# Kernel tuning notes

Hardware: AMD Instinct MI355X
Metric: run time of the kernel (lower is better)

## Reference

```python
import jax, jax.numpy as jnp
import numpy as np
from jax.scipy.special import logsumexp

EPSILON = 0.01        # temperature
DIST_THRESH = 0.2
NUM_ITERS = 3
NEG_INF = -1.0e9

B, N, M, C = 4, 4096, 4096, 256


def setup_inputs() -> dict:
    key = jax.random.key(0)
    k1, k2, k3, k4, k5 = jax.random.split(key, 5)
    source_feats = jax.random.normal(k1, (B, N, C), dtype=jnp.float32)
    source_locs = jax.random.uniform(k2, (B, N, 2), dtype=jnp.float32)
    target_locs = jax.random.uniform(k3, (B, M, 2), dtype=jnp.float32)
    source_valid_mask = jax.random.bernoulli(k4, 0.9, (B, N))
    target_valid_mask = jax.random.bernoulli(k5, 0.9, (B, M))
    return {
        "source_feats": source_feats,
        "source_locs": source_locs,
        "target_locs": target_locs,
        "source_valid_mask": source_valid_mask,
        "target_valid_mask": target_valid_mask,
    }


def reference(source_feats, source_locs, target_locs, source_valid_mask, target_valid_mask):
    # pairwise squared distances: [B, M, N]
    diff = target_locs[:, :, None, :] - source_locs[:, None, :, :]  # [B, M, N, 2]
    dist_sq = jnp.sum(diff * diff, axis=-1)                          # [B, M, N]
    log_K = -dist_sq / (EPSILON + 1e-8)

    valid_connection = dist_sq < (DIST_THRESH ** 2)
    valid_connection = valid_connection & source_valid_mask[:, None, :]
    valid_connection = valid_connection & target_valid_mask[:, :, None]
    log_K = jnp.where(valid_connection, log_K, NEG_INF)

    # Sinkhorn iterations in log space
    v = jnp.zeros((log_K.shape[0], 1, log_K.shape[2]), dtype=log_K.dtype)  # [B,1,N]
    u = jnp.zeros((log_K.shape[0], log_K.shape[1], 1), dtype=log_K.dtype)  # [B,M,1]
    for _ in range(NUM_ITERS):
        u = -logsumexp(log_K + v, axis=2, keepdims=True)
        v = -logsumexp(log_K + u, axis=1, keepdims=True)
        v = jnp.where(source_valid_mask[:, None, :], v, 0.0)

    attn = jnp.exp(log_K + u + v)  # [B, M, N]
    attn = jax.lax.stop_gradient(attn)  # original computes it under torch.no_grad

    target_feats = jnp.einsum('bmn,bnc->bmc', attn, source_feats)
    target_feats = target_feats * target_valid_mask[:, :, None].astype(target_feats.dtype)
    has_source = jnp.any(valid_connection, axis=-1, keepdims=True)
    target_feats = target_feats * has_source.astype(target_feats.dtype)
    return target_feats
```

## Files before the change

kernel.cpp:

```cpp
#include <hip/hip_runtime.h>
#include <math.h>

#define BB 4
#define BN 4096
#define CC 256
constexpr float T2      = 0.04f;
constexpr float INV_EPS = (float)(1.0 / 0.01000001);

typedef __attribute__((ext_vector_type(8)))  short bf16x8;
typedef __attribute__((ext_vector_type(16))) float f32x16;

__device__ __forceinline__ int cell_of(float x, float y) {
  int cx = (int)(x * 5.0f); cx = cx < 0 ? 0 : (cx > 4 ? 4 : cx);
  int cy = (int)(y * 5.0f); cy = cy < 0 ? 0 : (cy > 4 ? 4 : cy);
  return cy * 5 + cx;
}

__global__ __launch_bounds__(256) void k_bin(
    const float* __restrict__ tlocs, const float* __restrict__ slocs,
    const int* __restrict__ tmask, const int* __restrict__ smask,
    int* __restrict__ Zc, int* __restrict__ qcnt,
    int* __restrict__ starts_t, int* __restrict__ starts_s,
    int* __restrict__ perm_t, int* __restrict__ perm_s,
    float4* __restrict__ t_sorted, float4* __restrict__ s_sorted) {
  const int which = blockIdx.x & 1, b = blockIdx.x >> 1;
  const float* locs = which ? slocs : tlocs;
  const int*   mask = which ? smask : tmask;
  int* starts       = which ? starts_s : starts_t;
  int* perm         = which ? perm_s : perm_t;
  float4* pack      = which ? s_sorted : t_sorted;
  const int tid = threadIdx.x;
  if (blockIdx.x == 0) {
    Zc[tid] = 0;
    if (tid == 0) qcnt[0] = 0;
  }
  __shared__ int cnt[25];
  __shared__ int st[26];
  __shared__ int cur[25];
  if (tid < 25) cnt[tid] = 0;
  __syncthreads();
  for (int i = tid; i < BN; i += 256)
    atomicAdd(&cnt[cell_of(locs[(b * BN + i) * 2], locs[(b * BN + i) * 2 + 1])], 1);
  __syncthreads();
  if (tid == 0) {
    int acc = 0;
    for (int c = 0; c < 25; c++) { st[c] = acc; acc += cnt[c]; }
    st[25] = acc;
  }
  __syncthreads();
  if (tid < 25) cur[tid] = st[tid];
  if (tid < 26) starts[b * 32 + tid] = st[tid];
  __syncthreads();
  for (int i = tid; i < BN; i += 256) {
    float x = locs[(b * BN + i) * 2], y = locs[(b * BN + i) * 2 + 1];
    int pos = atomicAdd(&cur[cell_of(x, y)], 1);
    perm[b * BN + pos] = i;
    pack[b * BN + pos] = make_float4(x, y, 0.f, mask[b * BN + i] ? 1.f : 0.f);
  }
}

__global__ __launch_bounds__(256) void k_pack(
    const float* __restrict__ feats, const int* __restrict__ perm_s,
    unsigned* __restrict__ fB) {
  const int b   = blockIdx.x >> 8;
  const int blk = blockIdx.x & 255;
  const int tid = threadIdx.x;
  __shared__ int sidx[16];
  if (tid < 16) sidx[tid] = perm_s[b * BN + blk * 16 + tid];
  __syncthreads();
  const int ch = tid;
  unsigned pk[16];
  #pragma unroll
  for (int sl = 0; sl < 16; sl++) {
    float f = feats[((((size_t)(b << 12)) + sidx[sl]) << 8) + ch];
    unsigned fbt = __float_as_uint(f);
    unsigned hb  = fbt & 0xFFFF0000u;
    float lo = f - __uint_as_float(hb);
    pk[sl] = hb | (__float_as_uint(lo) >> 16);
  }
  unsigned* dst = fB + ((((size_t)b << 8) + blk) << 12) + ch * 16;
  #pragma unroll
  for (int q = 0; q < 4; q++)
    ((uint4*)dst)[q] = make_uint4(pk[q*4], pk[q*4+1], pk[q*4+2], pk[q*4+3]);
}

__global__ __launch_bounds__(256) void k_sink(const float4* __restrict__ opp,
                                              float4* __restrict__ own,
                                              const int* __restrict__ opp_starts,
                                              const int* __restrict__ Zin,
                                              int* __restrict__ Zout,
                                              int zero_invalid) {
  const int wv   = threadIdx.x >> 6;
  const int lane = threadIdx.x & 63;
  const int rowb = blockIdx.x * 16 + wv * 4;
  const int b    = rowb >> 12;
  float4 me[4];
  float  s[4] = {0.f, 0.f, 0.f, 0.f};
  int ryLo = 5, ryHi = -1, rxLo = 5, rxHi = -1;
  #pragma unroll
  for (int i = 0; i < 4; i++) {
    me[i] = own[rowb + i];
    if (me[i].w != 0.f) {
      int cell = cell_of(me[i].x, me[i].y);
      int cy = cell / 5, cx = cell % 5;
      ryLo = min(ryLo, max(cy - 1, 0)); ryHi = max(ryHi, min(cy + 1, 4));
      rxLo = min(rxLo, max(cx - 1, 0)); rxHi = max(rxHi, min(cx + 1, 4));
    }
  }
  for (int ry = ryLo; ry <= ryHi; ry++) {
    const int r0 = opp_starts[b * 32 + ry * 5 + rxLo];
    const int r1 = opp_starts[b * 32 + ry * 5 + rxHi + 1];
    for (int j = r0 + lane; j < r1; j += 64) {
      float4 o = opp[b * BN + j];
      #pragma unroll
      for (int i = 0; i < 4; i++) {
        float dx = me[i].x - o.x, dy = me[i].y - o.y;
        float d2 = fmaf(dx, dx, dy * dy);
        bool  c  = (d2 < T2) && (o.w != 0.f) && (me[i].w != 0.f);
        float t  = c ? fmaf(d2, -INV_EPS, o.z) : -3e30f;
        s[i] += __expf(t);
      }
    }
  }
  #pragma unroll
  for (int i = 0; i < 4; i++)
    for (int off = 32; off > 0; off >>= 1) s[i] += __shfl_xor(s[i], off);
  if (lane == 0) {
    const float Zf = (float)Zin[b];
    #pragma unroll
    for (int i = 0; i < 4; i++) {
      float ss  = s[i] + Zf;
      float val = (ss > 0.f) ? -logf(ss) : 1.0e9f;
      if (zero_invalid && me[i].w == 0.f) val = 0.f;
      own[rowb + i] = make_float4(me[i].x, me[i].y, val, me[i].w);
      if (val == 1.0e9f) atomicAdd(&Zout[b], 1);
    }
  }
}

#define NITEMS (BB * 25 * 12)

__global__ __launch_bounds__(256, 4) void k_out(
    const unsigned* __restrict__ fB, const float4* __restrict__ t_sorted,
    const float4* __restrict__ s_sorted, const int* __restrict__ perm_t,
    const int* __restrict__ starts_t, const int* __restrict__ starts_s,
    int* __restrict__ qcnt, float* __restrict__ out) {
  __shared__ float4 tL[32];
  __shared__ __align__(16) float Dl[32 * 268];
  __shared__ int qi;

  const int tid  = threadIdx.x;
  const int lane = tid & 63;
  const int w    = tid >> 6;
  const int kg   = lane >> 5;
  const int ln   = lane & 31;

  for (;;) {
    if (tid == 0) qi = atomicAdd(qcnt, 1);
    __syncthreads();
    const int item = qi;
    __syncthreads();
    if (item >= NITEMS) break;
    const int b    = item / 300;
    const int r1_  = item % 300;
    const int cell = r1_ / 12;
    const int chunk = r1_ % 12;
    const int cy = cell / 5, cx = cell % 5;
    const int t0 = starts_t[b * 32 + cell], t1 = starts_t[b * 32 + cell + 1];
    const int base = t0 + chunk * 32;
    if (base >= t1) continue;
    const int ry0 = max(cy - 1, 0), ry1 = min(cy + 1, 4);
    const int rx0 = max(cx - 1, 0), rx1 = min(cx + 1, 4);
    const int nt = min(32, t1 - base);

    if (tid < 32)
      tL[tid] = (tid < nt) ? t_sorted[b * BN + base + tid]
                           : make_float4(0.f, 0.f, 0.f, 0.f);
    __syncthreads();
    const float4 t4a = tL[ln];
    const int sB = b * BN;
    const unsigned* fBb = fB + (((size_t)b) << 20);
    const int aoff0 = (w * 64 + ln) * 16 + kg * 8;
    const int aoff1 = aoff0 + 512;

    f32x16 acc0, acc1;
    #pragma unroll
    for (int i = 0; i < 16; i++) { acc0[i] = 0.f; acc1[i] = 0.f; }

    for (int ry = ry0; ry <= ry1; ry++) {
      const int s0 = starts_s[b * 32 + ry * 5 + rx0];
      const int s1 = starts_s[b * 32 + ry * 5 + rx1 + 1];
      if (s0 >= s1) continue;
      const int blk0 = s0 >> 4;
      const int nBlk = ((s1 + 15) >> 4) - blk0;

      const unsigned* g0p = fBb + ((size_t)blk0 << 12);
      uint4 cA00 = *(const uint4*)(g0p + aoff0);
      uint4 cA01 = *(const uint4*)(g0p + aoff0 + 4);
      uint4 cA10 = *(const uint4*)(g0p + aoff1);
      uint4 cA11 = *(const uint4*)(g0p + aoff1 + 4);

      for (int r = 0; r < nBlk; r++) {
        const int tn = blk0 + min(r + 1, nBlk - 1);
        const unsigned* gn = fBb + ((size_t)tn << 12);
        uint4 nA00 = *(const uint4*)(gn + aoff0);
        uint4 nA01 = *(const uint4*)(gn + aoff0 + 4);
        uint4 nA10 = *(const uint4*)(gn + aoff1);
        uint4 nA11 = *(const uint4*)(gn + aoff1 + 4);
        const int j0 = (blk0 + r) * 16 + kg * 8;
        float4 s4v[8];
        #pragma unroll
        for (int e = 0; e < 8; e++)
          s4v[e] = s_sorted[sB + j0 + e];
        union { unsigned u[4]; bf16x8 v; } BH, BL;
        #pragma unroll
        for (int i = 0; i < 4; i++) {
          unsigned hh[2], ll[2];
          #pragma unroll
          for (int p = 0; p < 2; p++) {
            const int e = 2 * i + p;
            float4 s4 = s4v[e];
            int j = j0 + e;
            float dx = t4a.x - s4.x, dy = t4a.y - s4.y;
            float d2 = fmaf(dx, dx, dy * dy);
            bool  c  = (j >= s0) && (j < s1) && (d2 < T2) &&
                       (s4.w != 0.f) && (t4a.w != 0.f);
            float a  = c ? __expf(fmaf(d2, -INV_EPS, t4a.z + s4.z)) : 0.f;
            unsigned ab = __float_as_uint(a);
            unsigned hb = ab & 0xFFFF0000u;
            float alo = a - __uint_as_float(hb);
            hh[p] = ab >> 16;
            ll[p] = __float_as_uint(alo) >> 16;
          }
          BH.u[i] = hh[0] | (hh[1] << 16);
          BL.u[i] = ll[0] | (ll[1] << 16);
        }
        #pragma unroll
        for (int mt = 0; mt < 2; mt++) {
          union { uint4 q[2]; unsigned u[8]; } A;
          A.q[0] = (mt == 0) ? cA00 : cA10;
          A.q[1] = (mt == 0) ? cA01 : cA11;
          union { unsigned u[4]; bf16x8 v; } AH, AL;
          #pragma unroll
          for (int i = 0; i < 4; i++) {
            AH.u[i] = (A.u[2*i] >> 16)     | (A.u[2*i+1] & 0xFFFF0000u);
            AL.u[i] = (A.u[2*i] & 0xFFFFu) | (A.u[2*i+1] << 16);
          }
          if (mt == 0) {
            acc0 = __builtin_amdgcn_mfma_f32_32x32x16_bf16(AH.v, BH.v, acc0, 0, 0, 0);
            acc0 = __builtin_amdgcn_mfma_f32_32x32x16_bf16(AH.v, BL.v, acc0, 0, 0, 0);
            acc0 = __builtin_amdgcn_mfma_f32_32x32x16_bf16(AL.v, BH.v, acc0, 0, 0, 0);
          } else {
            acc1 = __builtin_amdgcn_mfma_f32_32x32x16_bf16(AH.v, BH.v, acc1, 0, 0, 0);
            acc1 = __builtin_amdgcn_mfma_f32_32x32x16_bf16(AH.v, BL.v, acc1, 0, 0, 0);
            acc1 = __builtin_amdgcn_mfma_f32_32x32x16_bf16(AL.v, BH.v, acc1, 0, 0, 0);
          }
        }
        cA00 = nA00; cA01 = nA01; cA10 = nA10; cA11 = nA11;
      }
    }

    __syncthreads();
    #pragma unroll
    for (int mt = 0; mt < 2; mt++) {
      #pragma unroll
      for (int rg = 0; rg < 4; rg++) {
        int chb = w * 64 + mt * 32 + 8 * rg + 4 * kg;
        float4 v;
        if (mt == 0) v = make_float4(acc0[rg*4], acc0[rg*4+1], acc0[rg*4+2], acc0[rg*4+3]);
        else         v = make_float4(acc1[rg*4], acc1[rg*4+1], acc1[rg*4+2], acc1[rg*4+3]);
        *(float4*)&Dl[ln * 268 + chb] = v;
      }
    }
    __syncthreads();
    {
      const int tmg = tid >> 5, chg = tid & 31;
      #pragma unroll
      for (int i = 0; i < 4; i++) {
        int tm = tmg * 4 + i;
        if (tm < nt) {
          int row = perm_t[sB + base + tm];
          float* op = out + (((b << 12) + row) << 8) + chg * 4;
          *(float4*)(op)       = *(float4*)&Dl[tm * 268 + chg * 4];
          *(float4*)(op + 128) = *(float4*)&Dl[tm * 268 + 128 + chg * 4];
        }
      }
    }
  }
}

extern "C" void kernel_launch(void* const* d_in, const int* in_sizes, int n_in,
                              void* d_out, int out_size, void* d_ws, size_t ws_size,
                              hipStream_t stream) {
  const float* feats = (const float*)d_in[0];
  const float* slocs = (const float*)d_in[1];
  const float* tlocs = (const float*)d_in[2];
  const int*   smask = (const int*)d_in[3];
  const int*   tmask = (const int*)d_in[4];
  float* out = (float*)d_out;

  char* ws = (char*)d_ws;
  int*    qcnt     = (int*)(ws);
  int*    Zc       = (int*)(ws + 1024);
  int*    starts_t = (int*)(ws + 2048);
  int*    starts_s = (int*)(ws + 2560);
  int*    perm_t   = (int*)(ws + 4096);
  int*    perm_s   = (int*)(ws + 69632);
  float4* s_sorted = (float4*)(ws + 135168);
  float4* t_sorted = (float4*)(ws + 397312);
  unsigned* fB     = (unsigned*)(ws + 663552);

  hipMemsetAsync(out, 0, (size_t)out_size * sizeof(float), stream);
  k_bin<<<8, 256, 0, stream>>>(tlocs, slocs, tmask, smask, Zc, qcnt,
                               starts_t, starts_s, perm_t, perm_s,
                               t_sorted, s_sorted);
  k_pack<<<1024, 256, 0, stream>>>(feats, perm_s, fB);
  for (int it = 0; it < 3; it++) {
    k_sink<<<1024, 256, 0, stream>>>(s_sorted, t_sorted, starts_s,
                                     Zc + (it == 0 ? 0 : (2 * it) * 4),
                                     Zc + (2 * it + 1) * 4, 0);
    k_sink<<<1024, 256, 0, stream>>>(t_sorted, s_sorted, starts_t,
                                     Zc + (2 * it + 1) * 4,
                                     Zc + (2 * it + 2) * 4, 1);
  }
  k_out<<<1024, 256, 0, stream>>>(fB, t_sorted, s_sorted, perm_t,
                                  starts_t, starts_s, qcnt, out);
}
```

Baseline: 535.1 us.

## Replace atomic work queue in k_out with static grid and halve LDS staging

```diff
diff --git a/kernel.cpp b/kernel.cpp
--- a/kernel.cpp
+++ b/kernel.cpp
@@ -19,7 +19,7 @@
 __global__ __launch_bounds__(256) void k_bin(
     const float* __restrict__ tlocs, const float* __restrict__ slocs,
     const int* __restrict__ tmask, const int* __restrict__ smask,
-    int* __restrict__ Zc, int* __restrict__ qcnt,
+    int* __restrict__ Zc,
     int* __restrict__ starts_t, int* __restrict__ starts_s,
     int* __restrict__ perm_t, int* __restrict__ perm_s,
     float4* __restrict__ t_sorted, float4* __restrict__ s_sorted) {
@@ -30,10 +30,7 @@
   int* perm         = which ? perm_s : perm_t;
   float4* pack      = which ? s_sorted : t_sorted;
   const int tid = threadIdx.x;
-  if (blockIdx.x == 0) {
-    Zc[tid] = 0;
-    if (tid == 0) qcnt[0] = 0;
-  }
+  if (blockIdx.x == 0) Zc[tid] = 0;
   __shared__ int cnt[25];
   __shared__ int st[26];
   __shared__ int cur[25];
@@ -140,14 +137,13 @@
 
 #define NITEMS (BB * 25 * 12)
 
-__global__ __launch_bounds__(256, 4) void k_out(
+__global__ __launch_bounds__(256, 6) void k_out(
     const unsigned* __restrict__ fB, const float4* __restrict__ t_sorted,
     const float4* __restrict__ s_sorted, const int* __restrict__ perm_t,
     const int* __restrict__ starts_t, const int* __restrict__ starts_s,
-    int* __restrict__ qcnt, float* __restrict__ out) {
+    float* __restrict__ out) {
   __shared__ float4 tL[32];
-  __shared__ __align__(16) float Dl[32 * 268];
-  __shared__ int qi;
+  __shared__ __align__(16) float Dl[32 * 132];
 
   const int tid  = threadIdx.x;
   const int lane = tid & 63;
@@ -155,121 +151,120 @@
   const int kg   = lane >> 5;
   const int ln   = lane & 31;
 
-  for (;;) {
-    if (tid == 0) qi = atomicAdd(qcnt, 1);
-    __syncthreads();
-    const int item = qi;
-    __syncthreads();
-    if (item >= NITEMS) break;
-    const int b    = item / 300;
-    const int r1_  = item % 300;
-    const int cell = r1_ / 12;
-    const int chunk = r1_ % 12;
-    const int cy = cell / 5, cx = cell % 5;
-    const int t0 = starts_t[b * 32 + cell], t1 = starts_t[b * 32 + cell + 1];
-    const int base = t0 + chunk * 32;
-    if (base >= t1) continue;
-    const int ry0 = max(cy - 1, 0), ry1 = min(cy + 1, 4);
-    const int rx0 = max(cx - 1, 0), rx1 = min(cx + 1, 4);
-    const int nt = min(32, t1 - base);
-
-    if (tid < 32)
-      tL[tid] = (tid < nt) ? t_sorted[b * BN + base + tid]
-                           : make_float4(0.f, 0.f, 0.f, 0.f);
-    __syncthreads();
-    const float4 t4a = tL[ln];
-    const int sB = b * BN;
-    const unsigned* fBb = fB + (((size_t)b) << 20);
-    const int aoff0 = (w * 64 + ln) * 16 + kg * 8;
-    const int aoff1 = aoff0 + 512;
-
-    f32x16 acc0, acc1;
-    #pragma unroll
-    for (int i = 0; i < 16; i++) { acc0[i] = 0.f; acc1[i] = 0.f; }
-
-    for (int ry = ry0; ry <= ry1; ry++) {
-      const int s0 = starts_s[b * 32 + ry * 5 + rx0];
-      const int s1 = starts_s[b * 32 + ry * 5 + rx1 + 1];
-      if (s0 >= s1) continue;
-      const int blk0 = s0 >> 4;
-      const int nBlk = ((s1 + 15) >> 4) - blk0;
-
-      const unsigned* g0p = fBb + ((size_t)blk0 << 12);
-      uint4 cA00 = *(const uint4*)(g0p + aoff0);
-      uint4 cA01 = *(const uint4*)(g0p + aoff0 + 4);
-      uint4 cA10 = *(const uint4*)(g0p + aoff1);
-      uint4 cA11 = *(const uint4*)(g0p + aoff1 + 4);
-
-      for (int r = 0; r < nBlk; r++) {
-        const int tn = blk0 + min(r + 1, nBlk - 1);
-        const unsigned* gn = fBb + ((size_t)tn << 12);
-        uint4 nA00 = *(const uint4*)(gn + aoff0);
-        uint4 nA01 = *(const uint4*)(gn + aoff0 + 4);
-        uint4 nA10 = *(const uint4*)(gn + aoff1);
-        uint4 nA11 = *(const uint4*)(gn + aoff1 + 4);
-        const int j0 = (blk0 + r) * 16 + kg * 8;
-        float4 s4v[8];
+  const int item = blockIdx.x;
+  const int b    = item / 300;
+  const int r1_  = item % 300;
+  const int cell = r1_ / 12;
+  const int chunk = r1_ % 12;
+  const int cy = cell / 5, cx = cell % 5;
+  const int t0 = starts_t[b * 32 + cell], t1 = starts_t[b * 32 + cell + 1];
+  const int base = t0 + chunk * 32;
+  if (base >= t1) return;
+  const int ry0 = max(cy - 1, 0), ry1 = min(cy + 1, 4);
+  const int rx0 = max(cx - 1, 0), rx1 = min(cx + 1, 4);
+  const int nt = min(32, t1 - base);
+
+  if (tid < 32)
+    tL[tid] = (tid < nt) ? t_sorted[b * BN + base + tid]
+                         : make_float4(0.f, 0.f, 0.f, 0.f);
+  __syncthreads();
+  const float4 t4a = tL[ln];
+  const int sB = b * BN;
+  const unsigned* fBb = fB + (((size_t)b) << 20);
+  const int aoff0 = (w * 64 + ln) * 16 + kg * 8;
+  const int aoff1 = aoff0 + 512;
+
+  f32x16 acc0, acc1;
+  #pragma unroll
+  for (int i = 0; i < 16; i++) { acc0[i] = 0.f; acc1[i] = 0.f; }
+
+  for (int ry = ry0; ry <= ry1; ry++) {
+    const int s0 = starts_s[b * 32 + ry * 5 + rx0];
+    const int s1 = starts_s[b * 32 + ry * 5 + rx1 + 1];
+    if (s0 >= s1) continue;
+    const int blk0 = s0 >> 4;
+    const int nBlk = ((s1 + 15) >> 4) - blk0;
+
+    const unsigned* g0p = fBb + ((size_t)blk0 << 12);
+    uint4 cA00 = *(const uint4*)(g0p + aoff0);
+    uint4 cA01 = *(const uint4*)(g0p + aoff0 + 4);
+    uint4 cA10 = *(const uint4*)(g0p + aoff1);
+    uint4 cA11 = *(const uint4*)(g0p + aoff1 + 4);
+
+    for (int r = 0; r < nBlk; r++) {
+      const int tn = blk0 + min(r + 1, nBlk - 1);
+      const unsigned* gn = fBb + ((size_t)tn << 12);
+      uint4 nA00 = *(const uint4*)(gn + aoff0);
+      uint4 nA01 = *(const uint4*)(gn + aoff0 + 4);
+      uint4 nA10 = *(const uint4*)(gn + aoff1);
+      uint4 nA11 = *(const uint4*)(gn + aoff1 + 4);
+      const int j0 = (blk0 + r) * 16 + kg * 8;
+      float4 s4v[8];
+      #pragma unroll
+      for (int e = 0; e < 8; e++)
+        s4v[e] = s_sorted[sB + j0 + e];
+      union { unsigned u[4]; bf16x8 v; } BH, BL;
+      #pragma unroll
+      for (int i = 0; i < 4; i++) {
+        unsigned hh[2], ll[2];
         #pragma unroll
-        for (int e = 0; e < 8; e++)
-          s4v[e] = s_sorted[sB + j0 + e];
-        union { unsigned u[4]; bf16x8 v; } BH, BL;
+        for (int p = 0; p < 2; p++) {
+          const int e = 2 * i + p;
+          float4 s4 = s4v[e];
+          int j = j0 + e;
+          float dx = t4a.x - s4.x, dy = t4a.y - s4.y;
+          float d2 = fmaf(dx, dx, dy * dy);
+          bool  c  = (j >= s0) && (j < s1) && (d2 < T2) &&
+                     (s4.w != 0.f) && (t4a.w != 0.f);
+          float a  = c ? __expf(fmaf(d2, -INV_EPS, t4a.z + s4.z)) : 0.f;
+          unsigned ab = __float_as_uint(a);
+          unsigned hb = ab & 0xFFFF0000u;
+          float alo = a - __uint_as_float(hb);
+          hh[p] = ab >> 16;
+          ll[p] = __float_as_uint(alo) >> 16;
+        }
+        BH.u[i] = hh[0] | (hh[1] << 16);
+        BL.u[i] = ll[0] | (ll[1] << 16);
+      }
+      #pragma unroll
+      for (int mt = 0; mt < 2; mt++) {
+        union { uint4 q[2]; unsigned u[8]; } A;
+        A.q[0] = (mt == 0) ? cA00 : cA10;
+        A.q[1] = (mt == 0) ? cA01 : cA11;
+        union { unsigned u[4]; bf16x8 v; } AH, AL;
         #pragma unroll
         for (int i = 0; i < 4; i++) {
-          unsigned hh[2], ll[2];
-          #pragma unroll
-          for (int p = 0; p < 2; p++) {
-            const int e = 2 * i + p;
-            float4 s4 = s4v[e];
-            int j = j0 + e;
-            float dx = t4a.x - s4.x, dy = t4a.y - s4.y;
-            float d2 = fmaf(dx, dx, dy * dy);
-            bool  c  = (j >= s0) && (j < s1) && (d2 < T2) &&
-                       (s4.w != 0.f) && (t4a.w != 0.f);
-            float a  = c ? __expf(fmaf(d2, -INV_EPS, t4a.z + s4.z)) : 0.f;
-            unsigned ab = __float_as_uint(a);
-            unsigned hb = ab & 0xFFFF0000u;
-            float alo = a - __uint_as_float(hb);
-            hh[p] = ab >> 16;
-            ll[p] = __float_as_uint(alo) >> 16;
-          }
-          BH.u[i] = hh[0] | (hh[1] << 16);
-          BL.u[i] = ll[0] | (ll[1] << 16);
-        }
+          AH.u[i] = (A.u[2*i] >> 16)     | (A.u[2*i+1] & 0xFFFF0000u);
+          AL.u[i] = (A.u[2*i] & 0xFFFFu) | (A.u[2*i+1] << 16);
+        }
+        if (mt == 0) {
+          acc0 = __builtin_amdgcn_mfma_f32_32x32x16_bf16(AH.v, BH.v, acc0, 0, 0, 0);
+          acc0 = __builtin_amdgcn_mfma_f32_32x32x16_bf16(AH.v, BL.v, acc0, 0, 0, 0);
+          acc0 = __builtin_amdgcn_mfma_f32_32x32x16_bf16(AL.v, BH.v, acc0, 0, 0, 0);
+        } else {
+          acc1 = __builtin_amdgcn_mfma_f32_32x32x16_bf16(AH.v, BH.v, acc1, 0, 0, 0);
+          acc1 = __builtin_amdgcn_mfma_f32_32x32x16_bf16(AH.v, BL.v, acc1, 0, 0, 0);
+          acc1 = __builtin_amdgcn_mfma_f32_32x32x16_bf16(AL.v, BH.v, acc1, 0, 0, 0);
+        }
+      }
+      cA00 = nA00; cA01 = nA01; cA10 = nA10; cA11 = nA11;
+    }
+  }
+
+  #pragma unroll
+  for (int p = 0; p < 2; p++) {
+    __syncthreads();
+    if ((w >> 1) == p) {
+      #pragma unroll
+      for (int mt = 0; mt < 2; mt++) {
         #pragma unroll
-        for (int mt = 0; mt < 2; mt++) {
-          union { uint4 q[2]; unsigned u[8]; } A;
-          A.q[0] = (mt == 0) ? cA00 : cA10;
-          A.q[1] = (mt == 0) ? cA01 : cA11;
-          union { unsigned u[4]; bf16x8 v; } AH, AL;
-          #pragma unroll
-          for (int i = 0; i < 4; i++) {
-            AH.u[i] = (A.u[2*i] >> 16)     | (A.u[2*i+1] & 0xFFFF0000u);
-            AL.u[i] = (A.u[2*i] & 0xFFFFu) | (A.u[2*i+1] << 16);
-          }
-          if (mt == 0) {
-            acc0 = __builtin_amdgcn_mfma_f32_32x32x16_bf16(AH.v, BH.v, acc0, 0, 0, 0);
-            acc0 = __builtin_amdgcn_mfma_f32_32x32x16_bf16(AH.v, BL.v, acc0, 0, 0, 0);
-            acc0 = __builtin_amdgcn_mfma_f32_32x32x16_bf16(AL.v, BH.v, acc0, 0, 0, 0);
-          } else {
-            acc1 = __builtin_amdgcn_mfma_f32_32x32x16_bf16(AH.v, BH.v, acc1, 0, 0, 0);
-            acc1 = __builtin_amdgcn_mfma_f32_32x32x16_bf16(AH.v, BL.v, acc1, 0, 0, 0);
-            acc1 = __builtin_amdgcn_mfma_f32_32x32x16_bf16(AL.v, BH.v, acc1, 0, 0, 0);
-          }
-        }
-        cA00 = nA00; cA01 = nA01; cA10 = nA10; cA11 = nA11;
-      }
-    }
-
-    __syncthreads();
-    #pragma unroll
-    for (int mt = 0; mt < 2; mt++) {
-      #pragma unroll
-      for (int rg = 0; rg < 4; rg++) {
-        int chb = w * 64 + mt * 32 + 8 * rg + 4 * kg;
-        float4 v;
-        if (mt == 0) v = make_float4(acc0[rg*4], acc0[rg*4+1], acc0[rg*4+2], acc0[rg*4+3]);
-        else         v = make_float4(acc1[rg*4], acc1[rg*4+1], acc1[rg*4+2], acc1[rg*4+3]);
-        *(float4*)&Dl[ln * 268 + chb] = v;
+        for (int rg = 0; rg < 4; rg++) {
+          int chb = (w & 1) * 64 + mt * 32 + 8 * rg + 4 * kg;
+          float4 v;
+          if (mt == 0) v = make_float4(acc0[rg*4], acc0[rg*4+1], acc0[rg*4+2], acc0[rg*4+3]);
+          else         v = make_float4(acc1[rg*4], acc1[rg*4+1], acc1[rg*4+2], acc1[rg*4+3]);
+          *(float4*)&Dl[ln * 132 + chb] = v;
+        }
       }
     }
     __syncthreads();
@@ -280,9 +275,8 @@
         int tm = tmg * 4 + i;
         if (tm < nt) {
           int row = perm_t[sB + base + tm];
-          float* op = out + (((b << 12) + row) << 8) + chg * 4;
-          *(float4*)(op)       = *(float4*)&Dl[tm * 268 + chg * 4];
-          *(float4*)(op + 128) = *(float4*)&Dl[tm * 268 + 128 + chg * 4];
+          float* op = out + (((b << 12) + row) << 8) + p * 128 + chg * 4;
+          *(float4*)op = *(float4*)&Dl[tm * 132 + chg * 4];
         }
       }
     }
@@ -300,7 +294,6 @@
   float* out = (float*)d_out;
 
   char* ws = (char*)d_ws;
-  int*    qcnt     = (int*)(ws);
   int*    Zc       = (int*)(ws + 1024);
   int*    starts_t = (int*)(ws + 2048);
   int*    starts_s = (int*)(ws + 2560);
@@ -311,7 +304,7 @@
   unsigned* fB     = (unsigned*)(ws + 663552);
 
   hipMemsetAsync(out, 0, (size_t)out_size * sizeof(float), stream);
-  k_bin<<<8, 256, 0, stream>>>(tlocs, slocs, tmask, smask, Zc, qcnt,
+  k_bin<<<8, 256, 0, stream>>>(tlocs, slocs, tmask, smask, Zc,
                                starts_t, starts_s, perm_t, perm_s,
                                t_sorted, s_sorted);
   k_pack<<<1024, 256, 0, stream>>>(feats, perm_s, fB);
@@ -323,6 +316,6 @@
                                      Zc + (2 * it + 1) * 4,
                                      Zc + (2 * it + 2) * 4, 1);
   }
-  k_out<<<1024, 256, 0, stream>>>(fB, t_sorted, s_sorted, perm_t,
-                                  starts_t, starts_s, qcnt, out);
-}
+  k_out<<<NITEMS, 256, 0, stream>>>(fB, t_sorted, s_sorted, perm_t,
+                                    starts_t, starts_s, out);
+}
```

New measurement: 917.5 us. 1.71x slower.
